# Optimization experiments

Hardware: AMD Instinct MI355X
Metric: run time of the kernel (lower is better)

## Reference

```python
import jax, jax.numpy as jnp
import numpy as np
import math

S, B, H, NH = 2048, 2, 2048, 16
HN = H // NH  # 128, head dim


def _rope_cache(seq_len, hn):
    # inv_freqs over even indices, half_hn entries
    inv_freqs = 0.0001 ** (jnp.arange(0, hn, 2, dtype=jnp.float32) / hn)
    pos = jnp.arange(seq_len, dtype=jnp.float32)
    angles = pos[:, None] * inv_freqs  # [s, hn/2]
    return jnp.cos(angles), jnp.sin(angles)


def _apply_rope(x, cos, sin):
    # x: [s, b, np, hn]; cos/sin: [s, hn/2] broadcast over b, np
    half = x.shape[-1] // 2
    c = cos[:, None, None, :]
    s = sin[:, None, None, :]
    left, right = x[..., :half], x[..., half:]
    return jnp.concatenate((c * left - s * right, s * left + c * right), axis=-1)


def setup_inputs() -> dict:
    key = jax.random.key(0)
    k0, k1, k2 = jax.random.split(key, 3)
    hidden_states = jax.random.normal(k0, (S, B, H), dtype=jnp.float32)
    # causal additive mask, broadcast over batch and heads
    causal = jnp.tril(jnp.ones((S, S), dtype=bool))
    attention_mask = jnp.where(causal, 0.0, -1e9).astype(jnp.float32)[None, None]
    W_qkv = jax.random.normal(k1, (3 * H, H), dtype=jnp.float32) * 0.02
    b_qkv = jnp.zeros((3 * H,), dtype=jnp.float32)
    W_dense = jax.random.normal(k2, (H, H), dtype=jnp.float32) * 0.02
    b_dense = jnp.zeros((H,), dtype=jnp.float32)
    return {"hidden_states": hidden_states, "attention_mask": attention_mask,
            "W_qkv": W_qkv, "b_qkv": b_qkv, "W_dense": W_dense, "b_dense": b_dense}


def reference(hidden_states, attention_mask, W_qkv, b_qkv, W_dense, b_dense):
    s, b, h = hidden_states.shape
    # fused QKV projection: [s,b,3h] -> [s,b,np,3*hn] -> split per head
    mixed = hidden_states @ W_qkv.T + b_qkv
    mixed = mixed.reshape(s, b, NH, 3 * HN)
    q, k, v = jnp.split(mixed, 3, axis=-1)  # each [s,b,np,hn]
    cos, sin = _rope_cache(s, HN)
    q = _apply_rope(q, cos, sin)
    k = _apply_rope(k, cos, sin)
    norm_factor = math.sqrt(HN)  # coeff is None (scale_attn_by_inverse_layer_idx=False)
    scores = jnp.einsum('sbnh,tbnh->bnst', q, k) / norm_factor  # [b,np,sq,sk]
    scores = scores + attention_mask
    probs = jax.nn.softmax(scores, axis=-1)  # dropout p=0 in eval
    ctx = jnp.einsum('bnst,tbnh->sbnh', probs, v).reshape(s, b, h)
    return ctx @ W_dense.T + b_dense  # [s,b,h]
```

## Files before the change

### kernel.cpp

```cpp
#include <hip/hip_runtime.h>

#define SEQ   2048
#define BATCH 2
#define HID   2048
#define NHEAD 16
#define HDIM  128
#define MTOT  4096
#define KDIM  2048

typedef __attribute__((ext_vector_type(8))) short  bf16x8;
typedef __attribute__((ext_vector_type(4))) float  f32x4;
typedef __attribute__((ext_vector_type(4))) unsigned short u16x4;
typedef __attribute__((ext_vector_type(8))) unsigned short u16x8;

__device__ __forceinline__ unsigned short f2bf(float x) {
  unsigned u = __float_as_uint(x);
  u += 0x7fffu + ((u >> 16) & 1u);
  return (unsigned short)(u >> 16);
}

__device__ __forceinline__ float fexp2(float x) {
  float r;
  asm("v_exp_f32 %0, %1" : "=v"(r) : "v"(x));
  return r;
}

__device__ __forceinline__ void gl_lds16(const void* g, void* l) {
  __builtin_amdgcn_global_load_lds(
      (__attribute__((address_space(1))) void*)g,
      (__attribute__((address_space(3))) void*)l, 16, 0, 0);
}

__device__ __forceinline__ f32x4 mfma16(bf16x8 a, bf16x8 b, f32x4 c) {
  return __builtin_amdgcn_mfma_f32_16x16x32_bf16(a, b, c, 0, 0, 0);
}

__global__ __launch_bounds__(256, 8)
void prep(const float* __restrict__ hidden, const float* __restrict__ Wqkv,
          const float* __restrict__ Wd,
          unsigned short* __restrict__ hidb, unsigned short* __restrict__ wqkvb,
          unsigned short* __restrict__ wdb,
          float* __restrict__ cosT, float* __restrict__ sinT) {
  int bid = blockIdx.x;
  if (bid < 24576) {
    const float* src; unsigned short* dst; int lb;
    if (bid < 8192)       { src = hidden; dst = hidb;  lb = bid; }
    else if (bid < 20480) { src = Wqkv;   dst = wqkvb; lb = bid - 8192; }
    else                  { src = Wd;     dst = wdb;   lb = bid - 20480; }
    int i = lb * 256 + threadIdx.x;
    int base = i << 2;
    int r = base >> 11, k = base & 2047;
    f32x4 v = *(const f32x4*)(src + base);
    int kp = k ^ (((r >> 1) & 7) << 3);
    u16x4 o;
    o[0] = f2bf(v[0]); o[1] = f2bf(v[1]); o[2] = f2bf(v[2]); o[3] = f2bf(v[3]);
    *(u16x4*)(dst + (size_t)r * 2048 + kp) = o;
  } else {
    int idx = (bid - 24576) * 256 + threadIdx.x;
    int s = idx >> 6, i = idx & 63;
    float inv = powf(1e-4f, (float)i * (1.0f / 64.0f));
    float a = (float)s * inv;
    cosT[idx] = cosf(a);
    sinT[idx] = sinf(a);
  }
}

__global__ __launch_bounds__(512, 2)
void gemm_qkv(const unsigned short* __restrict__ A,
              const unsigned short* __restrict__ Bt,
              const float* __restrict__ bias,
              unsigned short* __restrict__ Qs,
              unsigned short* __restrict__ Ks,
              unsigned short* __restrict__ Vt,
              const float* __restrict__ cosT,
              const float* __restrict__ sinT)
{
  __shared__ alignas(16) char lds[147456];
  const int tid = threadIdx.x;
  const int wid = tid >> 6, lane = tid & 63, g = lane >> 4, c = lane & 15;
  const int wr = wid >> 2, wc = wid & 3;

  const int bid = blockIdx.x;
  const int swz = (bid & 7) * 64 + (bid >> 3);
  const int nblk = swz & 15, mblk = swz >> 4;
  const int m0 = mblk << 7;
  const int n0 = nblk * 384;
  const int nh = nblk;

  char* ldsb = (char*)lds;
  const int sw = c >> 1;
  const char* ldsA0 = ldsb + (wr * 64 + c) * 128 + ((g ^ sw) << 4);
  const char* ldsA1 = ldsb + (wr * 64 + c) * 128 + (((4 + g) ^ sw) << 4);
  const char* ldsB0 = ldsb + 49152 + (wc * 16 + c) * 128 + ((g ^ sw) << 4);
  const char* ldsB1 = ldsb + 49152 + (wc * 16 + c) * 128 + (((4 + g) ^ sw) << 4);

  const char* gA = (const char*)A  + (size_t)(m0 + (tid >> 3)) * 4096 + (tid & 7) * 16;
  const char* gB = (const char*)Bt + (size_t)(n0 + (tid >> 3)) * 4096 + (tid & 7) * 16;
  char* lA = ldsb + tid * 16;
  char* lB = ldsb + 49152 + tid * 16;

#define STG_A(T, BUF) do { const char* _g = gA + (T) * 128; char* _l = lA + (BUF) * 16384; \
    gl_lds16(_g, _l); gl_lds16(_g + 262144, _l + 8192); } while (0)
#define STG_B(T, BUF) do { const char* _g = gB + (T) * 128; char* _l = lB + (BUF) * 49152; \
    gl_lds16(_g, _l);           gl_lds16(_g + 262144, _l + 8192);   \
    gl_lds16(_g + 524288, _l + 16384); gl_lds16(_g + 786432, _l + 24576); \
    gl_lds16(_g + 1048576, _l + 32768); gl_lds16(_g + 1310720, _l + 40960); } while (0)

  f32x4 acc[4][6];
#pragma unroll
  for (int i = 0; i < 4; ++i)
#pragma unroll
    for (int j = 0; j < 6; ++j) {
      acc[i][j][0] = 0.f; acc[i][j][1] = 0.f; acc[i][j][2] = 0.f; acc[i][j][3] = 0.f;
    }

  bf16x8 a0[4], a1[4], b0[6], b1[6];
  const int NT = KDIM / 64;

#define TILE(T, SA, SB) do {                                                \
    if ((T) + 1 < NT) { STG_B((T) + 1, ((T) + 1) & 1); }                    \
    if ((T) + 2 < NT) { STG_A((T) + 2, ((T) + 2) % 3); }                    \
    _Pragma("unroll")                                                       \
    for (int mf = 0; mf < 4; ++mf) {                                        \
      a0[mf] = *(const bf16x8*)(ldsA0 + (SA) * 16384 + mf * 2048);          \
      a1[mf] = *(const bf16x8*)(ldsA1 + (SA) * 16384 + mf * 2048);          \
    }                                                                       \
    _Pragma("unroll")                                                       \
    for (int nl = 0; nl < 6; ++nl) {                                        \
      b0[nl] = *(const bf16x8*)(ldsB0 + (SB) * 49152 + nl * 8192);          \
      b1[nl] = *(const bf16x8*)(ldsB1 + (SB) * 49152 + nl * 8192);          \
    }                                                                       \
    __builtin_amdgcn_s_setprio(1);                                          \
    _Pragma("unroll")                                                       \
    for (int mf = 0; mf < 4; ++mf)                                          \
      _Pragma("unroll")                                                     \
      for (int nl = 0; nl < 6; ++nl)                                        \
        acc[mf][nl] = mfma16(a0[mf], b0[nl], acc[mf][nl]);                  \
    _Pragma("unroll")                                                       \
    for (int mf = 0; mf < 4; ++mf)                                          \
      _Pragma("unroll")                                                     \
      for (int nl = 0; nl < 6; ++nl)                                        \
        acc[mf][nl] = mfma16(a1[mf], b1[nl], acc[mf][nl]);                  \
    __builtin_amdgcn_s_setprio(0);                                          \
    if ((T) + 2 < NT) { asm volatile("s_waitcnt vmcnt(2)" ::: "memory"); }  \
    else              { asm volatile("s_waitcnt vmcnt(0)" ::: "memory"); }  \
    __builtin_amdgcn_s_barrier();                                           \
  } while (0)

  STG_B(0, 0); STG_A(0, 0); STG_A(1, 1);
  asm volatile("s_waitcnt vmcnt(2)" ::: "memory");
  __builtin_amdgcn_s_barrier();

  for (int t = 0; t < 30; t += 6) {
    TILE(t + 0, 0, 0);
    TILE(t + 1, 1, 1);
    TILE(t + 2, 2, 0);
    TILE(t + 3, 0, 1);
    TILE(t + 4, 1, 0);
    TILE(t + 5, 2, 1);
  }
  TILE(30, 0, 0);
  TILE(31, 1, 1);

  const float qsc = 0.08838834764831845f * 1.4426950408889634f;
  const int dl = wc * 16 + c;
  unsigned short* Vtmp = (unsigned short*)ldsb;
  const int s0 = m0 >> 1;
#pragma unroll
  for (int ar = 0; ar < 4; ++ar) {
#pragma unroll
    for (int rr = 0; rr < 4; ++rr) {
      int m = m0 + wr * 64 + ar * 16 + g * 4 + rr;
      int s = m >> 1, bb = m & 1;
      size_t plane = (size_t)(bb * NHEAD + nh) * (SEQ * HDIM);
      int swb = (s & 7) << 3;
      float co = cosT[s * 64 + dl], si = sinT[s * 64 + dl];
      {
        float xl = acc[ar][0][rr] + bias[n0 + dl];
        float xr = acc[ar][1][rr] + bias[n0 + 64 + dl];
        Qs[plane + (size_t)s * HDIM + (dl ^ swb)]        = f2bf((co * xl - si * xr) * qsc);
        Qs[plane + (size_t)s * HDIM + ((dl + 64) ^ swb)] = f2bf((si * xl + co * xr) * qsc);
      }
      {
        float xl = acc[ar][2][rr] + bias[n0 + 128 + dl];
        float xr = acc[ar][3][rr] + bias[n0 + 192 + dl];
        Ks[plane + (size_t)s * HDIM + (dl ^ swb)]        = f2bf(co * xl - si * xr);
        Ks[plane + (size_t)s * HDIM + ((dl + 64) ^ swb)] = f2bf(si * xl + co * xr);
      }
      {
        int sloc = s - s0;
        Vtmp[(bb * 64 + sloc) * 136 + dl]      = f2bf(acc[ar][4][rr] + bias[n0 + 256 + dl]);
        Vtmp[(bb * 64 + sloc) * 136 + dl + 64] = f2bf(acc[ar][5][rr] + bias[n0 + 320 + dl]);
      }
    }
  }
  __syncthreads();
  {
    int b2 = tid >> 8, r = tid & 255;
    int d = r >> 1, half = r & 1;
    size_t planeV = (size_t)(b2 * NHEAD + nh) * (SEQ * HDIM);
    unsigned short* dstp = Vt + planeV + (size_t)d * SEQ + s0;
    int swb = (d & 7) << 3;
#pragma unroll
    for (int gg = 0; gg < 4; ++gg) {
      u16x8 v;
#pragma unroll
      for (int e = 0; e < 8; ++e)
        v[e] = Vtmp[(b2 * 64 + half * 32 + gg * 8 + e) * 136 + d];
      int tloc = half * 32 + gg * 8;
      *(u16x8*)(dstp + (tloc ^ swb)) = v;
    }
  }
#undef TILE
#undef STG_A
#undef STG_B
}

__global__ __launch_bounds__(512, 2)
void gemm_out(const unsigned short* __restrict__ A,
              const unsigned short* __restrict__ Bt,
              const float* __restrict__ bias,
              float* __restrict__ Cout)
{
  __shared__ alignas(16) char lds[147456];
  const int tid = threadIdx.x;
  const int wid = tid >> 6, lane = tid & 63, g = lane >> 4, c = lane & 15;
  const int wr = wid >> 2, wc = wid & 3;

  const int bid = blockIdx.x;
  const int swz = (bid & 7) * 32 + (bid >> 3);
  const int nblk = swz >> 5, mblk = swz & 31;
  const int m0 = mblk << 7, n0 = nblk << 8;

  char* ldsb = (char*)lds;
  const int sw = c >> 1;
  const char* ldsA0 = ldsb + (wr * 64 + c) * 128 + ((g ^ sw) << 4);
  const char* ldsA1 = ldsb + (wr * 64 + c) * 128 + (((4 + g) ^ sw) << 4);
  const char* ldsB0 = ldsb + 49152 + (wc * 64 + c) * 128 + ((g ^ sw) << 4);
  const char* ldsB1 = ldsb + 49152 + (wc * 64 + c) * 128 + (((4 + g) ^ sw) << 4);

  const char* gA = (const char*)A  + (size_t)(m0 + (tid >> 3)) * 4096 + (tid & 7) * 16;
  const char* gB = (const char*)Bt + (size_t)(n0 + (tid >> 3)) * 4096 + (tid & 7) * 16;
  char* lA = ldsb + tid * 16;
  char* lB = ldsb + 49152 + tid * 16;

#define STG_A(T, BUF) do { const char* _g = gA + (T) * 128; char* _l = lA + (BUF) * 16384; \
    gl_lds16(_g, _l); gl_lds16(_g + 262144, _l + 8192); } while (0)
#define STG_B(T, BUF) do { const char* _g = gB + (T) * 128; char* _l = lB + (BUF) * 32768; \
    gl_lds16(_g, _l);           gl_lds16(_g + 262144, _l + 8192);   \
    gl_lds16(_g + 524288, _l + 16384); gl_lds16(_g + 786432, _l + 24576); } while (0)

  f32x4 acc[4][4];
#pragma unroll
  for (int i = 0; i < 4; ++i)
#pragma unroll
    for (int j = 0; j < 4; ++j) {
      acc[i][j][0] = 0.f; acc[i][j][1] = 0.f; acc[i][j][2] = 0.f; acc[i][j][3] = 0.f;
    }

  bf16x8 a0[4], a1[4], b0[4], b1[4];
  const int NT = KDIM / 64;

#define TILE(T, S) do {                                                     \
    if ((T) + 2 < NT) { STG_B((T) + 2, ((T) + 2) % 3); STG_A((T) + 2, ((T) + 2) % 3); } \
    _Pragma("unroll")                                                       \
    for (int mf = 0; mf < 4; ++mf) {                                        \
      a0[mf] = *(const bf16x8*)(ldsA0 + (S) * 16384 + mf * 2048);           \
      a1[mf] = *(const bf16x8*)(ldsA1 + (S) * 16384 + mf * 2048);           \
    }                                                                       \
    _Pragma("unroll")                                                       \
    for (int nl = 0; nl < 4; ++nl) {                                        \
      b0[nl] = *(const bf16x8*)(ldsB0 + (S) * 32768 + nl * 2048);           \
      b1[nl] = *(const bf16x8*)(ldsB1 + (S) * 32768 + nl * 2048);           \
    }                                                                       \
    __builtin_amdgcn_s_setprio(1);                                          \
    _Pragma("unroll")                                                       \
    for (int mf = 0; mf < 4; ++mf)                                          \
      _Pragma("unroll")                                                     \
      for (int nl = 0; nl < 4; ++nl)                                        \
        acc[mf][nl] = mfma16(a0[mf], b0[nl], acc[mf][nl]);                  \
    _Pragma("unroll")                                                       \
    for (int mf = 0; mf < 4; ++mf)                                          \
      _Pragma("unroll")                                                     \
      for (int nl = 0; nl < 4; ++nl)                                        \
        acc[mf][nl] = mfma16(a1[mf], b1[nl], acc[mf][nl]);                  \
    __builtin_amdgcn_s_setprio(0);                                          \
    if ((T) + 2 < NT) { asm volatile("s_waitcnt vmcnt(6)" ::: "memory"); }  \
    else              { asm volatile("s_waitcnt vmcnt(0)" ::: "memory"); }  \
    __builtin_amdgcn_s_barrier();                                           \
  } while (0)

  STG_B(0, 0); STG_A(0, 0);
  STG_B(1, 1); STG_A(1, 1);
  asm volatile("s_waitcnt vmcnt(6)" ::: "memory");
  __builtin_amdgcn_s_barrier();

  for (int t = 0; t < 30; t += 3) {
    TILE(t, 0);
    TILE(t + 1, 1);
    TILE(t + 2, 2);
  }
  TILE(30, 0);
  TILE(31, 1);

#pragma unroll
  for (int mf = 0; mf < 4; ++mf)
#pragma unroll
    for (int rr = 0; rr < 4; ++rr) {
      int m = m0 + wr * 64 + mf * 16 + g * 4 + rr;
#pragma unroll
      for (int nl = 0; nl < 4; ++nl) {
        int n = n0 + wc * 64 + nl * 16 + c;
        Cout[(size_t)m * HID + n] = acc[mf][nl][rr] + bias[n];
      }
    }
#undef TILE
#undef STG_A
#undef STG_B
}

__global__ __launch_bounds__(512, 2)
void attn(const unsigned short* __restrict__ Qs,
          const unsigned short* __restrict__ Ks,
          const unsigned short* __restrict__ Vt,
          unsigned short* __restrict__ ctx)
{
  __shared__ alignas(16) unsigned short Klds[2][64 * 128];
  __shared__ alignas(16) unsigned short Vlds[128 * 64];
  __shared__ alignas(16) unsigned short Plds[256 * 72];
  const int tid = threadIdx.x;
  const int w = tid >> 6, lane = tid & 63, g = lane >> 4, c = lane & 15;
  const int bid = blockIdx.x;
  const int head = bid & 31;
  const int j = bid >> 5;
  const int qbh = 15 - j;
  const int q0w = (w < 4) ? ((qbh << 7) + w * 32) : ((j << 7) + (w - 4) * 32);
  const size_t plane = (size_t)head * (SEQ * HDIM);
  const unsigned short* Qp = Qs + plane;

  bf16x8 qf[2][4];
#pragma unroll
  for (int q2 = 0; q2 < 2; ++q2) {
    int s = q0w + q2 * 16 + c;
    int swb = (s & 7) << 3;
#pragma unroll
    for (int kk = 0; kk < 4; ++kk) {
      int d0 = kk * 32 + g * 8;
      qf[q2][kk] = *(const bf16x8*)(Qp + (size_t)s * HDIM + (d0 ^ swb));
    }
  }

  f32x4 accO[2][8];
#pragma unroll
  for (int i = 0; i < 2; ++i)
#pragma unroll
    for (int jj = 0; jj < 8; ++jj) {
      accO[i][jj][0] = 0.f; accO[i][jj][1] = 0.f; accO[i][jj][2] = 0.f; accO[i][jj][3] = 0.f;
    }
  float mrun[2] = { -1e30f, -1e30f };
  float lrun[2] = { 0.f, 0.f };

  const char* Kg = (const char*)(Ks + plane) + (tid >> 4) * 256 + (tid & 15) * 16;
  const char* Vg = (const char*)(Vt + plane) + (size_t)(tid >> 3) * 4096 + (tid & 7) * 16;

  const int ntiles = (qbh << 1) + 2;
  const int qminw = q0w;
  const int qmaxw = q0w + 31;

  gl_lds16(Kg,        (char*)Klds[0] + tid * 16);
  gl_lds16(Kg + 8192, (char*)Klds[0] + tid * 16 + 8192);

  for (int kt = 0; kt < ntiles; ++kt) {
    const int t0 = kt << 6;
    const bool havenext = (kt + 1 < ntiles);

    gl_lds16(Vg + t0 * 2,          (char*)Vlds + tid * 16);
    gl_lds16(Vg + t0 * 2 + 262144, (char*)Vlds + tid * 16 + 8192);
    if (havenext) {
      char* kd = (char*)Klds[(kt + 1) & 1] + tid * 16;
      gl_lds16(Kg + (size_t)(t0 + 64) * 256,        kd);
      gl_lds16(Kg + (size_t)(t0 + 64) * 256 + 8192, kd + 8192);
    }
    if (havenext) asm volatile("s_waitcnt vmcnt(4)" ::: "memory");
    else          asm volatile("s_waitcnt vmcnt(2)" ::: "memory");
    __builtin_amdgcn_s_barrier();

    if (t0 <= qmaxw) {
      const char* Kb = (const char*)Klds[kt & 1];
      f32x4 sacc[4][2];
#pragma unroll
      for (int i = 0; i < 4; ++i)
#pragma unroll
        for (int jj = 0; jj < 2; ++jj) {
          sacc[i][jj][0] = 0.f; sacc[i][jj][1] = 0.f; sacc[i][jj][2] = 0.f; sacc[i][jj][3] = 0.f;
        }
      __builtin_amdgcn_s_setprio(1);
#pragma unroll
      for (int kk = 0; kk < 4; ++kk) {
        bf16x8 kf[4];
#pragma unroll
        for (int ta = 0; ta < 4; ++ta) {
          int t = ta * 16 + c;
          int d0 = kk * 32 + g * 8;
          kf[ta] = *(const bf16x8*)(Kb + t * 256 + ((d0 ^ ((t & 7) << 3)) << 1));
        }
#pragma unroll
        for (int ta = 0; ta < 4; ++ta)
#pragma unroll
          for (int q2 = 0; q2 < 2; ++q2)
            sacc[ta][q2] = mfma16(kf[ta], qf[q2][kk], sacc[ta][q2]);
      }
      __builtin_amdgcn_s_setprio(0);

      if (t0 + 63 > qminw) {
#pragma unroll
        for (int ta = 0; ta < 4; ++ta)
#pragma unroll
          for (int q2 = 0; q2 < 2; ++q2)
#pragma unroll
            for (int r = 0; r < 4; ++r) {
              int t = t0 + ta * 16 + g * 4 + r;
              int q = qminw + q2 * 16 + c;
              if (t > q) sacc[ta][q2][r] = -30000.f;
            }
      }

      float corr[2];
      bool resc = false;
#pragma unroll
      for (int q2 = 0; q2 < 2; ++q2) {
        float mx = -30000.f;
#pragma unroll
        for (int ta = 0; ta < 4; ++ta)
          mx = fmaxf(mx, fmaxf(fmaxf(sacc[ta][q2][0], sacc[ta][q2][1]),
                               fmaxf(sacc[ta][q2][2], sacc[ta][q2][3])));
        mx = fmaxf(mx, __shfl_xor(mx, 16));
        mx = fmaxf(mx, __shfl_xor(mx, 32));
        bool rs = mx > mrun[q2] + 8.0f;
        resc |= rs;
        float mnew = rs ? mx : mrun[q2];
        corr[q2] = fexp2(mrun[q2] - mnew);
        mrun[q2] = mnew;
        float ls = 0.f;
#pragma unroll
        for (int ta = 0; ta < 4; ++ta)
#pragma unroll
          for (int r = 0; r < 4; ++r) {
            float e = fexp2(sacc[ta][q2][r] - mnew);
            sacc[ta][q2][r] = e;
            ls += e;
          }
        ls += __shfl_xor(ls, 16);
        ls += __shfl_xor(ls, 32);
        lrun[q2] = lrun[q2] * corr[q2] + ls;
      }

      if (__any(resc)) {
#pragma unroll
        for (int q2 = 0; q2 < 2; ++q2)
#pragma unroll
          for (int r = 0; r < 4; ++r) {
            float cD = __shfl(corr[q2], (lane & 48) | (((lane >> 4) << 2) + r));
#pragma unroll
            for (int fn = 0; fn < 8; ++fn) accO[q2][fn][r] *= cD;
          }
      }

#pragma unroll
      for (int q2 = 0; q2 < 2; ++q2) {
        int prow = w * 32 + q2 * 16 + c;
#pragma unroll
        for (int ta = 0; ta < 4; ++ta) {
          u16x4 pk;
          pk[0] = f2bf(sacc[ta][q2][0]); pk[1] = f2bf(sacc[ta][q2][1]);
          pk[2] = f2bf(sacc[ta][q2][2]); pk[3] = f2bf(sacc[ta][q2][3]);
          *(u16x4*)(&Plds[prow * 72 + ta * 16 + g * 4]) = pk;
        }
      }
    }

    if (havenext) asm volatile("s_waitcnt vmcnt(2)" ::: "memory");
    else          asm volatile("s_waitcnt vmcnt(0)" ::: "memory");
    __builtin_amdgcn_s_barrier();

    if (t0 <= qmaxw) {
      __builtin_amdgcn_s_setprio(1);
#pragma unroll
      for (int kk = 0; kk < 2; ++kk) {
        bf16x8 pa[2];
#pragma unroll
        for (int q2 = 0; q2 < 2; ++q2)
          pa[q2] = *(const bf16x8*)((const char*)Plds + (w * 32 + q2 * 16 + c) * 144 + (kk * 32 + g * 8) * 2);
#pragma unroll
        for (int fn = 0; fn < 8; ++fn) {
          int d = fn * 16 + c;
          int tt = kk * 32 + g * 8;
          bf16x8 vb = *(const bf16x8*)((const char*)Vlds + d * 128 + ((tt ^ ((d & 7) << 3)) << 1));
#pragma unroll
          for (int q2 = 0; q2 < 2; ++q2)
            accO[q2][fn] = mfma16(pa[q2], vb, accO[q2][fn]);
        }
      }
      __builtin_amdgcn_s_setprio(0);
    }
    __builtin_amdgcn_s_barrier();
  }

  const int b = head >> 4, nh = head & 15;
  float linv[2] = { 1.0f / lrun[0], 1.0f / lrun[1] };
#pragma unroll
  for (int q2 = 0; q2 < 2; ++q2)
#pragma unroll
    for (int r = 0; r < 4; ++r) {
      float inv = __shfl(linv[q2], (lane & 48) | (((lane >> 4) << 2) + r));
      int q = q0w + q2 * 16 + g * 4 + r;
      int m = q * 2 + b;
      int swb = ((m >> 1) & 7) << 3;
#pragma unroll
      for (int fn = 0; fn < 8; ++fn) {
        int h = nh * 128 + fn * 16 + c;
        ctx[(size_t)m * HID + (h ^ swb)] = f2bf(accO[q2][fn][r] * inv);
      }
    }
}

extern "C" void kernel_launch(void* const* d_in, const int* in_sizes, int n_in,
                              void* d_out, int out_size, void* d_ws, size_t ws_size,
                              hipStream_t stream) {
  const float* hidden = (const float*)d_in[0];
  const float* Wqkv = (const float*)d_in[2];
  const float* bqkv = (const float*)d_in[3];
  const float* Wd   = (const float*)d_in[4];
  const float* bd   = (const float*)d_in[5];
  float* out = (float*)d_out;
  char* ws = (char*)d_ws;

  const size_t OFF_HID  = 0;
  const size_t OFF_WQKV = 16777216;
  const size_t OFF_WD   = 41943040;
  const size_t OFF_COS  = 50331648;
  const size_t OFF_SIN  = 50855936;
  const size_t OFF_Q    = 51380224;
  const size_t OFF_K    = 68157440;
  const size_t OFF_VT   = 84934656;
  if (ws_size < 101711872) return;

  unsigned short* hidb  = (unsigned short*)(ws + OFF_HID);
  unsigned short* wqkvb = (unsigned short*)(ws + OFF_WQKV);
  unsigned short* wdb   = (unsigned short*)(ws + OFF_WD);
  float* cosT = (float*)(ws + OFF_COS);
  float* sinT = (float*)(ws + OFF_SIN);
  unsigned short* Qsb = (unsigned short*)(ws + OFF_Q);
  unsigned short* Ksb = (unsigned short*)(ws + OFF_K);
  unsigned short* Vtb = (unsigned short*)(ws + OFF_VT);
  unsigned short* ctxb = hidb;

  prep<<<25088, 256, 0, stream>>>(hidden, Wqkv, Wd, hidb, wqkvb, wdb, cosT, sinT);

  gemm_qkv<<<512, 512, 0, stream>>>(hidb, wqkvb, bqkv, Qsb, Ksb, Vtb, cosT, sinT);
  attn<<<256, 512, 0, stream>>>(Qsb, Ksb, Vtb, ctxb);
  gemm_out<<<256, 512, 0, stream>>>(ctxb, wdb, bd, out);
}
```

Before: 230.3 us.

## Double attention key/value tile to 128 and process P·V in two halves

The attention kernel now stages 128 keys per iteration instead of 64, with larger K double-buffers and V tiles in LDS, and half as many loop iterations. Per iteration the P·V step is split into two 64-key halves that reuse the same P scratch buffer. Each wave writes and reads only its own P rows, so the halves are separated by an LDS wait rather than a block barrier. This is meant to cut barriers and global-load issue overhead per key, at the cost of more LDS, more score registers, and more wasted masked work on the causal diagonal tiles.

```diff
diff --git a/kernel.cpp b/kernel.cpp
--- a/kernel.cpp
+++ b/kernel.cpp
@@ -325,8 +325,8 @@
           const unsigned short* __restrict__ Vt,
           unsigned short* __restrict__ ctx)
 {
-  __shared__ alignas(16) unsigned short Klds[2][64 * 128];
-  __shared__ alignas(16) unsigned short Vlds[128 * 64];
+  __shared__ alignas(16) unsigned short Klds[2][128 * 128];
+  __shared__ alignas(16) unsigned short Vlds[128 * 128];
   __shared__ alignas(16) unsigned short Plds[256 * 72];
   const int tid = threadIdx.x;
   const int w = tid >> 6, lane = tid & 63, g = lane >> 4, c = lane & 15;
@@ -361,35 +361,38 @@
   float lrun[2] = { 0.f, 0.f };
 
   const char* Kg = (const char*)(Ks + plane) + (tid >> 4) * 256 + (tid & 15) * 16;
-  const char* Vg = (const char*)(Vt + plane) + (size_t)(tid >> 3) * 4096 + (tid & 7) * 16;
-
-  const int ntiles = (qbh << 1) + 2;
+  const char* Vg = (const char*)(Vt + plane) + (size_t)(tid >> 4) * 4096 + (tid & 15) * 16;
+
+  const int ntiles = 16 - j;
   const int qminw = q0w;
   const int qmaxw = q0w + 31;
 
-  gl_lds16(Kg,        (char*)Klds[0] + tid * 16);
-  gl_lds16(Kg + 8192, (char*)Klds[0] + tid * 16 + 8192);
+#define STG_K(T, BUF) do { char* _kd = (char*)Klds[BUF] + tid * 16;            \
+    const char* _kg = Kg + (size_t)(T) * 32768;                                \
+    gl_lds16(_kg, _kd);              gl_lds16(_kg + 8192,  _kd + 8192);        \
+    gl_lds16(_kg + 16384, _kd + 16384); gl_lds16(_kg + 24576, _kd + 24576); } while (0)
+#define STG_V(T) do { char* _vd = (char*)Vlds + tid * 16;                      \
+    const char* _vg = Vg + (T) * 256;                                          \
+    gl_lds16(_vg, _vd);                gl_lds16(_vg + 131072, _vd + 8192);     \
+    gl_lds16(_vg + 262144, _vd + 16384); gl_lds16(_vg + 393216, _vd + 24576); } while (0)
+
+  STG_K(0, 0);
 
   for (int kt = 0; kt < ntiles; ++kt) {
-    const int t0 = kt << 6;
+    const int t0 = kt << 7;
     const bool havenext = (kt + 1 < ntiles);
 
-    gl_lds16(Vg + t0 * 2,          (char*)Vlds + tid * 16);
-    gl_lds16(Vg + t0 * 2 + 262144, (char*)Vlds + tid * 16 + 8192);
-    if (havenext) {
-      char* kd = (char*)Klds[(kt + 1) & 1] + tid * 16;
-      gl_lds16(Kg + (size_t)(t0 + 64) * 256,        kd);
-      gl_lds16(Kg + (size_t)(t0 + 64) * 256 + 8192, kd + 8192);
-    }
-    if (havenext) asm volatile("s_waitcnt vmcnt(4)" ::: "memory");
-    else          asm volatile("s_waitcnt vmcnt(2)" ::: "memory");
+    STG_V(kt);
+    if (havenext) STG_K(kt + 1, (kt + 1) & 1);
+    if (havenext) asm volatile("s_waitcnt vmcnt(8)" ::: "memory");
+    else          asm volatile("s_waitcnt vmcnt(4)" ::: "memory");
     __builtin_amdgcn_s_barrier();
 
     if (t0 <= qmaxw) {
       const char* Kb = (const char*)Klds[kt & 1];
-      f32x4 sacc[4][2];
-#pragma unroll
-      for (int i = 0; i < 4; ++i)
+      f32x4 sacc[8][2];
+#pragma unroll
+      for (int i = 0; i < 8; ++i)
 #pragma unroll
         for (int jj = 0; jj < 2; ++jj) {
           sacc[i][jj][0] = 0.f; sacc[i][jj][1] = 0.f; sacc[i][jj][2] = 0.f; sacc[i][jj][3] = 0.f;
@@ -397,24 +400,24 @@
       __builtin_amdgcn_s_setprio(1);
 #pragma unroll
       for (int kk = 0; kk < 4; ++kk) {
-        bf16x8 kf[4];
-#pragma unroll
-        for (int ta = 0; ta < 4; ++ta) {
+        bf16x8 kf[8];
+#pragma unroll
+        for (int ta = 0; ta < 8; ++ta) {
           int t = ta * 16 + c;
           int d0 = kk * 32 + g * 8;
           kf[ta] = *(const bf16x8*)(Kb + t * 256 + ((d0 ^ ((t & 7) << 3)) << 1));
         }
 #pragma unroll
-        for (int ta = 0; ta < 4; ++ta)
+        for (int ta = 0; ta < 8; ++ta)
 #pragma unroll
           for (int q2 = 0; q2 < 2; ++q2)
             sacc[ta][q2] = mfma16(kf[ta], qf[q2][kk], sacc[ta][q2]);
       }
       __builtin_amdgcn_s_setprio(0);
 
-      if (t0 + 63 > qminw) {
-#pragma unroll
-        for (int ta = 0; ta < 4; ++ta)
+      if (t0 + 127 > qminw) {
+#pragma unroll
+        for (int ta = 0; ta < 8; ++ta)
 #pragma unroll
           for (int q2 = 0; q2 < 2; ++q2)
 #pragma unroll
@@ -431,7 +434,7 @@
       for (int q2 = 0; q2 < 2; ++q2) {
         float mx = -30000.f;
 #pragma unroll
-        for (int ta = 0; ta < 4; ++ta)
+        for (int ta = 0; ta < 8; ++ta)
           mx = fmaxf(mx, fmaxf(fmaxf(sacc[ta][q2][0], sacc[ta][q2][1]),
                                fmaxf(sacc[ta][q2][2], sacc[ta][q2][3])));
         mx = fmaxf(mx, __shfl_xor(mx, 16));
@@ -443,7 +446,7 @@
         mrun[q2] = mnew;
         float ls = 0.f;
 #pragma unroll
-        for (int ta = 0; ta < 4; ++ta)
+        for (int ta = 0; ta < 8; ++ta)
 #pragma unroll
           for (int r = 0; r < 4; ++r) {
             float e = fexp2(sacc[ta][q2][r] - mnew);
@@ -466,45 +469,53 @@
           }
       }
 
-#pragma unroll
-      for (int q2 = 0; q2 < 2; ++q2) {
-        int prow = w * 32 + q2 * 16 + c;
-#pragma unroll
-        for (int ta = 0; ta < 4; ++ta) {
-          u16x4 pk;
-          pk[0] = f2bf(sacc[ta][q2][0]); pk[1] = f2bf(sacc[ta][q2][1]);
-          pk[2] = f2bf(sacc[ta][q2][2]); pk[3] = f2bf(sacc[ta][q2][3]);
-          *(u16x4*)(&Plds[prow * 72 + ta * 16 + g * 4]) = pk;
+      if (havenext) asm volatile("s_waitcnt vmcnt(4)" ::: "memory");
+      else          asm volatile("s_waitcnt vmcnt(0)" ::: "memory");
+      __builtin_amdgcn_s_barrier();
+
+#pragma unroll
+      for (int h = 0; h < 2; ++h) {
+#pragma unroll
+        for (int q2 = 0; q2 < 2; ++q2) {
+          int prow = w * 32 + q2 * 16 + c;
+#pragma unroll
+          for (int t4 = 0; t4 < 4; ++t4) {
+            u16x4 pk;
+            pk[0] = f2bf(sacc[h * 4 + t4][q2][0]); pk[1] = f2bf(sacc[h * 4 + t4][q2][1]);
+            pk[2] = f2bf(sacc[h * 4 + t4][q2][2]); pk[3] = f2bf(sacc[h * 4 + t4][q2][3]);
+            *(u16x4*)(&Plds[prow * 72 + t4 * 16 + g * 4]) = pk;
+          }
         }
-      }
-    }
-
-    if (havenext) asm volatile("s_waitcnt vmcnt(2)" ::: "memory");
-    else          asm volatile("s_waitcnt vmcnt(0)" ::: "memory");
+        asm volatile("s_waitcnt lgkmcnt(0)" ::: "memory");
+        __builtin_amdgcn_sched_barrier(0);
+        __builtin_amdgcn_s_setprio(1);
+#pragma unroll
+        for (int kk = 0; kk < 2; ++kk) {
+          bf16x8 pa[2];
+#pragma unroll
+          for (int q2 = 0; q2 < 2; ++q2)
+            pa[q2] = *(const bf16x8*)((const char*)Plds + (w * 32 + q2 * 16 + c) * 144 + (kk * 32 + g * 8) * 2);
+#pragma unroll
+          for (int fn = 0; fn < 8; ++fn) {
+            int d = fn * 16 + c;
+            int tt = h * 64 + kk * 32 + g * 8;
+            bf16x8 vb = *(const bf16x8*)((const char*)Vlds + d * 256 + ((tt ^ ((d & 7) << 3)) << 1));
+#pragma unroll
+            for (int q2 = 0; q2 < 2; ++q2)
+              accO[q2][fn] = mfma16(pa[q2], vb, accO[q2][fn]);
+          }
+        }
+        __builtin_amdgcn_s_setprio(0);
+      }
+    } else {
+      if (havenext) asm volatile("s_waitcnt vmcnt(4)" ::: "memory");
+      else          asm volatile("s_waitcnt vmcnt(0)" ::: "memory");
+      __builtin_amdgcn_s_barrier();
+    }
     __builtin_amdgcn_s_barrier();
-
-    if (t0 <= qmaxw) {
-      __builtin_amdgcn_s_setprio(1);
-#pragma unroll
-      for (int kk = 0; kk < 2; ++kk) {
-        bf16x8 pa[2];
-#pragma unroll
-        for (int q2 = 0; q2 < 2; ++q2)
-          pa[q2] = *(const bf16x8*)((const char*)Plds + (w * 32 + q2 * 16 + c) * 144 + (kk * 32 + g * 8) * 2);
-#pragma unroll
-        for (int fn = 0; fn < 8; ++fn) {
-          int d = fn * 16 + c;
-          int tt = kk * 32 + g * 8;
-          bf16x8 vb = *(const bf16x8*)((const char*)Vlds + d * 128 + ((tt ^ ((d & 7) << 3)) << 1));
-#pragma unroll
-          for (int q2 = 0; q2 < 2; ++q2)
-            accO[q2][fn] = mfma16(pa[q2], vb, accO[q2][fn]);
-        }
-      }
-      __builtin_amdgcn_s_setprio(0);
-    }
-    __builtin_amdgcn_s_barrier();
-  }
+  }
+#undef STG_K
+#undef STG_V
 
   const int b = head >> 4, nh = head & 15;
   float linv[2] = { 1.0f / lrun[0], 1.0f / lrun[1] };
```

Result: faster. 224.6 us (-2.5%).
